# Optimization experiments

Measured on AMD Instinct MI355X. Metric: run time of the kernel, lower is better.

The kernel has to match this reference:

```python
import jax, jax.numpy as jnp
import numpy as np
import math

B, S, H, NH, DH, FF, L = 2, 1024, 768, 12, 64, 3072, 4
LN_EPS = 1e-12


def _layer_norm(x, g, b):
    m = jnp.mean(x, axis=-1, keepdims=True)
    v = jnp.mean(jnp.square(x - m), axis=-1, keepdims=True)
    return (x - m) * jax.lax.rsqrt(v + LN_EPS) * g + b


def _gelu(x):
    # BERT erf-based gelu: x * 0.5 * (1 + erf(x / sqrt(2)))
    return x * 0.5 * (1.0 + jax.lax.erf(x / jnp.sqrt(jnp.asarray(2.0, x.dtype))))


def setup_inputs() -> dict:
    key = jax.random.key(0)
    ks = jax.random.split(key, 10)
    init = lambda k, shape: (jax.random.normal(k, shape, jnp.float32) * 0.02)
    inp = {
        'x': jax.random.normal(ks[0], (B, S, H), jnp.float32),
        'mask': jax.random.randint(ks[1], (B, S, S), 0, 2).astype(jnp.int32),
        'Wq': init(ks[2], (L, H, H)), 'bq': jnp.zeros((L, H), jnp.float32),
        'Wk': init(ks[3], (L, H, H)), 'bk': jnp.zeros((L, H), jnp.float32),
        'Wv': init(ks[4], (L, H, H)), 'bv': jnp.zeros((L, H), jnp.float32),
        'Wao': init(ks[5], (L, H, H)), 'bao': jnp.zeros((L, H), jnp.float32),
        'g1': jnp.ones((L, H), jnp.float32), 'b1': jnp.zeros((L, H), jnp.float32),
        'Wi': init(ks[6], (L, H, FF)), 'bi': jnp.zeros((L, FF), jnp.float32),
        'Wfo': init(ks[7], (L, FF, H)), 'bfo': jnp.zeros((L, H), jnp.float32),
        'g2': jnp.ones((L, H), jnp.float32), 'b2': jnp.zeros((L, H), jnp.float32),
    }
    return inp


def reference(x, mask, Wq, bq, Wk, bk, Wv, bv, Wao, bao, g1, b1, Wi, bi, Wfo, bfo, g2, b2):
    # additive mask: (1 - mask) * -10000, broadcast over heads -> [B,1,S,S]
    adder = (1.0 - mask.astype(x.dtype))[:, None, :, :] * -10000.0
    scale = 1.0 / math.sqrt(DH)

    def block(h, p):
        (wq, bq_, wk, bk_, wv, bv_, wao, bao_, g1_, b1_, wi, bi_, wfo, bfo_, g2_, b2_) = p
        q = (h @ wq + bq_).reshape(B, S, NH, DH)
        k = (h @ wk + bk_).reshape(B, S, NH, DH)
        v = (h @ wv + bv_).reshape(B, S, NH, DH)
        scores = jnp.einsum('bqhd,bkhd->bhqk', q, k) * scale + adder
        probs = jax.nn.softmax(scores, axis=-1)
        ctx = jnp.einsum('bhqk,bkhd->bqhd', probs, v).reshape(B, S, H)
        attn_out = _layer_norm(ctx @ wao + bao_ + h, g1_, b1_)
        inter = _gelu(attn_out @ wi + bi_)
        out = _layer_norm(inter @ wfo + bfo_ + attn_out, g2_, b2_)
        return out, None

    params = (Wq, bq, Wk, bk, Wv, bv, Wao, bao, g1, b1, Wi, bi, Wfo, bfo, g2, b2)
    out, _ = jax.lax.scan(block, x, params)
    return out
```

## Files before the change

kernel.cpp:

```cpp
#include <hip/hip_runtime.h>
#include <math.h>

#define B_  2
#define S_  1024
#define H_  768
#define NH_ 12
#define DH_ 64
#define FF_ 3072
#define L_  4

typedef short v8s __attribute__((ext_vector_type(8)));
typedef float v4f __attribute__((ext_vector_type(4)));

static __device__ __forceinline__ unsigned short f2bf(float f) {
    unsigned int u = __float_as_uint(f);
    unsigned int r = (u + 0x7fffu + ((u >> 16) & 1u)) >> 16;
    return (unsigned short)r;
}
static __device__ __forceinline__ float bf2f(unsigned short u) {
    return __uint_as_float((unsigned int)u << 16);
}

#define GLOAD16(g, l) __builtin_amdgcn_global_load_lds( \
    (const __attribute__((address_space(1))) unsigned int*)(g), \
    (__attribute__((address_space(3))) unsigned int*)(l), 16, 0, 0)

__global__ void conv_bf16_k(const float* __restrict__ in, unsigned short* __restrict__ out, int n) {
    int i = blockIdx.x * 256 + threadIdx.x;
    if (i < n) out[i] = f2bf(in[i]);
}

__global__ void maskconv_k(const int* __restrict__ m, unsigned short* __restrict__ o, int n) {
    int i = blockIdx.x * 256 + threadIdx.x;
    if (i < n) o[i] = m[i] ? (unsigned short)0u : (unsigned short)0xC61Cu;
}

__global__ __launch_bounds__(256) void transpose_convert(
    const float* __restrict__ W, unsigned short* __restrict__ Wt,
    int K, int N, size_t in_lstride, size_t out_lstride)
{
    __shared__ float tile[32][33];
    const int l = blockIdx.z;
    const float* src = W + (size_t)l * in_lstride;
    unsigned short* dst = Wt + (size_t)l * out_lstride;
    const int k0 = blockIdx.x * 32;
    const int n0 = blockIdx.y * 32;
    const int t = threadIdx.x;
    const int tc = t & 31, tr = t >> 5;
#pragma unroll
    for (int i = 0; i < 4; ++i) {
        int r = tr + i * 8;
        tile[r][tc] = src[(size_t)(k0 + r) * N + n0 + tc];
    }
    __syncthreads();
#pragma unroll
    for (int i = 0; i < 4; ++i) {
        int r = tr + i * 8;
        dst[(size_t)(n0 + r) * K + k0 + tc] = f2bf(tile[tc][r]);
    }
}

template<int ACT, int OUT_BF, int NBIAS, int SPLIT>
__global__ __launch_bounds__(256) void gemm_k(
    const unsigned short* __restrict__ A,
    const unsigned short* __restrict__ Bt,
    const float* __restrict__ b0,
    const float* __restrict__ b1,
    const float* __restrict__ b2,
    const float* __restrict__ res,
    void* __restrict__ out0,
    float* __restrict__ out1,
    int M, int N, int K, int klen)
{
    __shared__ __align__(16) unsigned short As[2][128 * 64];
    __shared__ __align__(16) unsigned short Bs[2][64 * 64];
    const int t = threadIdx.x;
    const int m0 = blockIdx.x * 128;
    const int n0 = blockIdx.y * 64;
    const int kz = SPLIT ? blockIdx.z : 0;
    const int kstart = kz * klen;
    const int lane = t & 63;
    const int w = t >> 6;
    const int wm = w >> 1, wn = w & 1;
    const int l15 = lane & 15;
    const int q4  = lane >> 4;

    const unsigned short* gA[4];
    const unsigned short* gB[2];
#pragma unroll
    for (int i = 0; i < 4; ++i) {
        int c = t + i * 256;
        int r = c >> 3, cc = c & 7;
        gA[i] = A + (size_t)(m0 + r) * K + kstart + ((cc ^ (r & 7)) << 3);
    }
#pragma unroll
    for (int i = 0; i < 2; ++i) {
        int c = t + i * 256;
        int r = c >> 3, cc = c & 7;
        gB[i] = Bt + (size_t)(n0 + r) * K + kstart + ((cc ^ (r & 7)) << 3);
    }
    const int ldsW = w * 512;

    v4f acc[4][2] = {};
    const int nt = klen >> 6;

#pragma unroll
    for (int i = 0; i < 4; ++i) GLOAD16(gA[i], &As[0][i * 2048 + ldsW]);
#pragma unroll
    for (int i = 0; i < 2; ++i) GLOAD16(gB[i], &Bs[0][i * 2048 + ldsW]);

    int cur = 0;
    for (int kt = 0; kt < nt; ++kt) {
        __syncthreads();
        if (kt + 1 < nt) {
            const size_t go = (size_t)(kt + 1) << 6;
#pragma unroll
            for (int i = 0; i < 4; ++i) GLOAD16(gA[i] + go, &As[cur ^ 1][i * 2048 + ldsW]);
#pragma unroll
            for (int i = 0; i < 2; ++i) GLOAD16(gB[i] + go, &Bs[cur ^ 1][i * 2048 + ldsW]);
        }
        const unsigned short* as = As[cur];
        const unsigned short* bs = Bs[cur];
#pragma unroll
        for (int ks = 0; ks < 2; ++ks) {
            v8s af[4], bf[2];
#pragma unroll
            for (int i = 0; i < 4; ++i) {
                int r = wm * 64 + i * 16 + l15;
                af[i] = *(const v8s*)&as[r * 64 + ((((ks << 2) + q4) ^ (r & 7)) << 3)];
            }
#pragma unroll
            for (int i = 0; i < 2; ++i) {
                int r = wn * 32 + i * 16 + l15;
                bf[i] = *(const v8s*)&bs[r * 64 + ((((ks << 2) + q4) ^ (r & 7)) << 3)];
            }
#pragma unroll
            for (int fm = 0; fm < 4; ++fm)
#pragma unroll
                for (int fn = 0; fn < 2; ++fn)
                    acc[fm][fn] = __builtin_amdgcn_mfma_f32_16x16x32_bf16(af[fm], bf[fn], acc[fm][fn], 0, 0, 0);
        }
        cur ^= 1;
    }

    const int rb = q4 * 4;
#pragma unroll
    for (int fm = 0; fm < 4; ++fm)
#pragma unroll
        for (int fn = 0; fn < 2; ++fn)
#pragma unroll
            for (int i = 0; i < 4; ++i) {
                const int row = m0 + wm * 64 + fm * 16 + rb + i;
                const int col = n0 + wn * 32 + fn * 16 + l15;
                float v = acc[fm][fn][i];
                const size_t oi = (size_t)row * N + col;
                if (!SPLIT || kz == 0) {
                    float bb;
                    if (NBIAS == 3) {
                        int which = (col >= 1536) ? 2 : (col >= 768 ? 1 : 0);
                        const float* bp = (which == 0) ? b0 : ((which == 1) ? b1 : b2);
                        bb = bp[col - which * 768];
                    } else {
                        bb = b0[col];
                    }
                    v += bb;
                    if (res) v += res[oi];
                    if (ACT == 1) v = 0.5f * v * (1.0f + erff(v * 0.70710678118654752f));
                    if (OUT_BF) ((unsigned short*)out0)[oi] = f2bf(v);
                    else        ((float*)out0)[oi] = v;
                } else {
                    out1[oi] = v;
                }
            }
}

__global__ __launch_bounds__(256) void ln_k(
    const float* __restrict__ ina, const float* __restrict__ inb,
    const float* __restrict__ g, const float* __restrict__ be,
    float* __restrict__ outf, unsigned short* __restrict__ outb)
{
    const int row = blockIdx.x;
    const float* xa = ina + (size_t)row * H_;
    const float* xb = inb + (size_t)row * H_;
    const int t = threadIdx.x;
    const int wave = t >> 6, lane = t & 63;
    float v0 = xa[t] + xb[t];
    float v1 = xa[t + 256] + xb[t + 256];
    float v2 = xa[t + 512] + xb[t + 512];
    float s = v0 + v1 + v2;
    float s2 = v0 * v0 + v1 * v1 + v2 * v2;
#pragma unroll
    for (int o = 32; o; o >>= 1) { s += __shfl_xor(s, o); s2 += __shfl_xor(s2, o); }
    __shared__ float rs[4], rq[4];
    if (lane == 0) { rs[wave] = s; rq[wave] = s2; }
    __syncthreads();
    s  = rs[0] + rs[1] + rs[2] + rs[3];
    s2 = rq[0] + rq[1] + rq[2] + rq[3];
    const float mean = s * (1.0f / 768.0f);
    float var = s2 * (1.0f / 768.0f) - mean * mean;
    var = fmaxf(var, 0.0f);
    const float inv = rsqrtf(var + 1e-12f);
#pragma unroll
    for (int i = 0; i < 3; ++i) {
        int c = t + i * 256;
        float vv = (i == 0) ? v0 : ((i == 1) ? v1 : v2);
        float y = (vv - mean) * inv * g[c] + be[c];
        outf[(size_t)row * H_ + c] = y;
        outb[(size_t)row * H_ + c] = f2bf(y);
    }
}

__global__ __launch_bounds__(512) void fattn_k(
    const unsigned short* __restrict__ qkv,
    const unsigned short* __restrict__ madd,
    unsigned short* __restrict__ ctx)
{
    const int qt = blockIdx.x, h = blockIdx.y, b = blockIdx.z;
    const int q0 = qt * 64;
    const int t = threadIdx.x;
    const int w = t >> 6, lane = t & 63;
    const int half = w >> 2, w4 = w & 3;
    const int l15 = lane & 15;
    const int kr8 = (lane >> 4) * 8;
    const int rb  = (lane >> 4) * 4;
    const int wq0 = w4 * 16;

    __shared__ __align__(16) unsigned char smem[53248];
    unsigned short* KsH = (unsigned short*)(smem)         + (size_t)half * (64 * 72);
    unsigned short* VtH = (unsigned short*)(smem + 18432) + (size_t)half * 4096;
    unsigned short* PsH = (unsigned short*)(smem + 34816) + (size_t)half * (64 * 72);

    const size_t rstr = 2304;
    const unsigned short* base = qkv + (size_t)b * S_ * rstr + h * 64;

    v8s qf0, qf1;
    {
        const unsigned short* qp = base + (size_t)(q0 + wq0 + l15) * rstr + kr8;
        qf0 = *(const v8s*)qp;
        qf1 = *(const v8s*)(qp + 32);
    }

    const int tl  = t & 255;
    const int skp = tl >> 3;
    const int sd0 = (tl & 7) * 8;
    const unsigned short* kbase = base + 768  + (size_t)(half * 512 + skp) * rstr + sd0;
    const unsigned short* vbase = base + 1536 + (size_t)(half * 512 + 2 * skp) * rstr + sd0;
    const size_t kstep = (size_t)64 * rstr;

    float m_[4], l_[4];
    v4f accO[4];
#pragma unroll
    for (int i = 0; i < 4; ++i) { m_[i] = -3.0e38f; l_[i] = 0.f; }
#pragma unroll
    for (int f = 0; f < 4; ++f) accO[f] = (v4f){0.f, 0.f, 0.f, 0.f};

    const unsigned short* mrow[4];
#pragma unroll
    for (int i = 0; i < 4; ++i)
        mrow[i] = madd + ((size_t)(b * S_) + q0 + wq0 + rb + i) * S_ + half * 512;

    v8s kA0, kA1, vA0, vA1, kB0, kB1, vB0, vB1;
    kA0 = *(const v8s*)(kbase);
    kA1 = *(const v8s*)(kbase + 32 * rstr);
    vA0 = *(const v8s*)(vbase);
    vA1 = *(const v8s*)(vbase + rstr);

    for (int kt = 0; kt < 8; ++kt) {
        const int k0 = kt * 64;
        __syncthreads();
        if ((kt & 1) == 0) {
            *(v8s*)&KsH[skp * 72 + sd0] = kA0;
            *(v8s*)&KsH[(skp + 32) * 72 + sd0] = kA1;
#pragma unroll
            for (int j = 0; j < 8; ++j) {
                const int d = sd0 + j;
                const int sw = ((d & 7) ^ (d >> 3)) << 3;
                unsigned int pk = ((unsigned int)(unsigned short)vA1[j] << 16) | (unsigned short)vA0[j];
                *(unsigned int*)&VtH[(size_t)d * 64 + ((2 * skp) ^ sw)] = pk;
            }
            if (kt < 7) {
                const unsigned short* kp = kbase + (size_t)(kt + 1) * kstep;
                const unsigned short* vp = vbase + (size_t)(kt + 1) * kstep;
                kB0 = *(const v8s*)kp;
                kB1 = *(const v8s*)(kp + 32 * rstr);
                vB0 = *(const v8s*)vp;
                vB1 = *(const v8s*)(vp + rstr);
            }
        } else {
            *(v8s*)&KsH[skp * 72 + sd0] = kB0;
            *(v8s*)&KsH[(skp + 32) * 72 + sd0] = kB1;
#pragma unroll
            for (int j = 0; j < 8; ++j) {
                const int d = sd0 + j;
                const int sw = ((d & 7) ^ (d >> 3)) << 3;
                unsigned int pk = ((unsigned int)(unsigned short)vB1[j] << 16) | (unsigned short)vB0[j];
                *(unsigned int*)&VtH[(size_t)d * 64 + ((2 * skp) ^ sw)] = pk;
            }
            if (kt < 7) {
                const unsigned short* kp = kbase + (size_t)(kt + 1) * kstep;
                const unsigned short* vp = vbase + (size_t)(kt + 1) * kstep;
                kA0 = *(const v8s*)kp;
                kA1 = *(const v8s*)(kp + 32 * rstr);
                vA0 = *(const v8s*)vp;
                vA1 = *(const v8s*)(vp + rstr);
            }
        }
        __syncthreads();

        v4f s4[4];
#pragma unroll
        for (int f = 0; f < 4; ++f) s4[f] = (v4f){0.f, 0.f, 0.f, 0.f};
#pragma unroll
        for (int ks = 0; ks < 2; ++ks) {
            v8s qv = ks ? qf1 : qf0;
#pragma unroll
            for (int f = 0; f < 4; ++f) {
                v8s kf = *(const v8s*)&KsH[(f * 16 + l15) * 72 + ks * 32 + kr8];
                s4[f] = __builtin_amdgcn_mfma_f32_16x16x32_bf16(qv, kf, s4[f], 0, 0, 0);
            }
        }

        float p[4][4];
        float mx[4];
#pragma unroll
        for (int i = 0; i < 4; ++i) mx[i] = -3.0e38f;
#pragma unroll
        for (int f = 0; f < 4; ++f)
#pragma unroll
            for (int i = 0; i < 4; ++i) {
                float v = s4[f][i] * 0.125f + bf2f(mrow[i][k0 + f * 16 + l15]);
                p[f][i] = v;
                mx[i] = fmaxf(mx[i], v);
            }
#pragma unroll
        for (int o = 8; o; o >>= 1)
#pragma unroll
            for (int i = 0; i < 4; ++i) mx[i] = fmaxf(mx[i], __shfl_xor(mx[i], o));
        float corr[4], rsum[4];
#pragma unroll
        for (int i = 0; i < 4; ++i) {
            float mn = fmaxf(m_[i], mx[i]);
            corr[i] = __expf(m_[i] - mn);
            m_[i] = mn;
            rsum[i] = 0.f;
        }
#pragma unroll
        for (int f = 0; f < 4; ++f)
#pragma unroll
            for (int i = 0; i < 4; ++i) {
                float e = __expf(p[f][i] - m_[i]);
                p[f][i] = e;
                rsum[i] += e;
            }
#pragma unroll
        for (int o = 8; o; o >>= 1)
#pragma unroll
            for (int i = 0; i < 4; ++i) rsum[i] += __shfl_xor(rsum[i], o);
#pragma unroll
        for (int i = 0; i < 4; ++i) l_[i] = l_[i] * corr[i] + rsum[i];
#pragma unroll
        for (int f = 0; f < 4; ++f)
#pragma unroll
            for (int i = 0; i < 4; ++i) accO[f][i] *= corr[i];

#pragma unroll
        for (int f = 0; f < 4; ++f)
#pragma unroll
            for (int i = 0; i < 4; ++i)
                PsH[(wq0 + rb + i) * 72 + f * 16 + l15] = f2bf(p[f][i]);

#pragma unroll
        for (int ks = 0; ks < 2; ++ks) {
            v8s pf = *(const v8s*)&PsH[(wq0 + l15) * 72 + ks * 32 + kr8];
#pragma unroll
            for (int f = 0; f < 4; ++f) {
                const int d = f * 16 + l15;
                const int sw = ((d & 7) ^ (d >> 3)) << 3;
                v8s vf = *(const v8s*)&VtH[(size_t)d * 64 + ((ks * 32 + kr8) ^ sw)];
                accO[f] = __builtin_amdgcn_mfma_f32_16x16x32_bf16(pf, vf, accO[f], 0, 0, 0);
            }
        }
    }

    __syncthreads();
    float* Mb = (float*)smem;
    const int mstr = 26;
    if (half == 1) {
        float* p = Mb + ((size_t)(w4 * 64 + lane)) * mstr;
#pragma unroll
        for (int i = 0; i < 4; ++i) { p[i] = m_[i]; p[4 + i] = l_[i]; }
#pragma unroll
        for (int f = 0; f < 4; ++f)
#pragma unroll
            for (int i = 0; i < 4; ++i) p[8 + f * 4 + i] = accO[f][i];
    }
    __syncthreads();
    if (half == 0) {
        const float* p = Mb + ((size_t)(w4 * 64 + lane)) * mstr;
        float c0[4], c1[4];
#pragma unroll
        for (int i = 0; i < 4; ++i) {
            float m1 = p[i], l1 = p[4 + i];
            float mm = fmaxf(m_[i], m1);
            c0[i] = __expf(m_[i] - mm);
            c1[i] = __expf(m1 - mm);
            l_[i] = l_[i] * c0[i] + l1 * c1[i];
            m_[i] = mm;
        }
#pragma unroll
        for (int f = 0; f < 4; ++f)
#pragma unroll
            for (int i = 0; i < 4; ++i) {
                float o = (accO[f][i] * c0[i] + p[8 + f * 4 + i] * c1[i]) / l_[i];
                size_t row = (size_t)(b * S_) + q0 + wq0 + rb + i;
                ctx[row * 768 + h * 64 + f * 16 + l15] = f2bf(o);
            }
    }
}

extern "C" void kernel_launch(void* const* d_in, const int* in_sizes, int n_in,
                              void* d_out, int out_size, void* d_ws, size_t ws_size,
                              hipStream_t stream)
{
    const float* x   = (const float*)d_in[0];
    const int*   mask= (const int*)  d_in[1];
    const float* Wq  = (const float*)d_in[2];
    const float* bq  = (const float*)d_in[3];
    const float* Wk  = (const float*)d_in[4];
    const float* bk  = (const float*)d_in[5];
    const float* Wv  = (const float*)d_in[6];
    const float* bv  = (const float*)d_in[7];
    const float* Wao = (const float*)d_in[8];
    const float* bao = (const float*)d_in[9];
    const float* g1  = (const float*)d_in[10];
    const float* b1  = (const float*)d_in[11];
    const float* Wi  = (const float*)d_in[12];
    const float* bi  = (const float*)d_in[13];
    const float* Wfo = (const float*)d_in[14];
    const float* bfo = (const float*)d_in[15];
    const float* g2  = (const float*)d_in[16];
    const float* b2  = (const float*)d_in[17];
    float* out = (float*)d_out;

    const int M = B_ * S_;
    char* basep = (char*)d_ws;
    size_t off = 0;
    auto alloc = [&](size_t bytes) -> char* {
        char* p = basep + off;
        off = (off + bytes + 255) & ~(size_t)255;
        return p;
    };

    unsigned short* WqkvT = (unsigned short*)alloc((size_t)L_ * 2304 * 768 * 2);
    unsigned short* WaoT  = (unsigned short*)alloc((size_t)L_ * 768 * 768 * 2);
    unsigned short* WiT   = (unsigned short*)alloc((size_t)L_ * 3072 * 768 * 2);
    unsigned short* WfoT  = (unsigned short*)alloc((size_t)L_ * 768 * 3072 * 2);
    unsigned short* h_bf  = (unsigned short*)alloc((size_t)M * 768 * 2);
    unsigned short* qkvbf = (unsigned short*)alloc((size_t)M * 2304 * 2);
    unsigned short* ctxbf = (unsigned short*)alloc((size_t)M * 768 * 2);
    float* t1a            = (float*)alloc((size_t)M * 768 * 4);
    float* attnf          = (float*)alloc((size_t)M * 768 * 4);
    unsigned short* attnbf= (unsigned short*)alloc((size_t)M * 768 * 2);
    unsigned short* interbf = (unsigned short*)alloc((size_t)M * FF_ * 2);
    unsigned short* madd  = (unsigned short*)alloc((size_t)B_ * S_ * S_ * 2);
    float* t1b = (float*)(void*)qkvbf;

    dim3 tb(256);
    transpose_convert<<<dim3(24, 24, L_), tb, 0, stream>>>(Wq,  WqkvT + 0,          768,  768, (size_t)768 * 768,  (size_t)2304 * 768);
    transpose_convert<<<dim3(24, 24, L_), tb, 0, stream>>>(Wk,  WqkvT + 768 * 768,  768,  768, (size_t)768 * 768,  (size_t)2304 * 768);
    transpose_convert<<<dim3(24, 24, L_), tb, 0, stream>>>(Wv,  WqkvT + 1536 * 768, 768,  768, (size_t)768 * 768,  (size_t)2304 * 768);
    transpose_convert<<<dim3(24, 24, L_), tb, 0, stream>>>(Wao, WaoT,               768,  768, (size_t)768 * 768,  (size_t)768 * 768);
    transpose_convert<<<dim3(24, 96, L_), tb, 0, stream>>>(Wi,  WiT,                768, 3072, (size_t)768 * 3072, (size_t)3072 * 768);
    transpose_convert<<<dim3(96, 24, L_), tb, 0, stream>>>(Wfo, WfoT,              3072,  768, (size_t)3072 * 768, (size_t)768 * 3072);

    conv_bf16_k<<<(M * 768 + 255) / 256, 256, 0, stream>>>(x, h_bf, M * 768);
    maskconv_k<<<(B_ * S_ * S_ + 255) / 256, 256, 0, stream>>>(mask, madd, B_ * S_ * S_);

    const float* hres = x;
    for (int l = 0; l < L_; ++l) {
        gemm_k<0, 1, 3, 0><<<dim3(16, 36), tb, 0, stream>>>(
            h_bf, WqkvT + (size_t)l * 2304 * 768,
            bq + l * 768, bk + l * 768, bv + l * 768, nullptr, qkvbf, nullptr, M, 2304, 768, 768);
        fattn_k<<<dim3(S_ / 64, NH_, B_), dim3(512), 0, stream>>>(qkvbf, madd, ctxbf);
        gemm_k<0, 0, 1, 1><<<dim3(16, 12, 2), tb, 0, stream>>>(
            ctxbf, WaoT + (size_t)l * 768 * 768,
            bao + l * 768, nullptr, nullptr, hres, t1a, t1b, M, 768, 768, 384);
        ln_k<<<M, tb, 0, stream>>>(t1a, t1b, g1 + l * 768, b1 + l * 768, attnf, attnbf);
        gemm_k<1, 1, 1, 0><<<dim3(16, 48), tb, 0, stream>>>(
            attnbf, WiT + (size_t)l * 3072 * 768,
            bi + l * 3072, nullptr, nullptr, nullptr, interbf, nullptr, M, 3072, 768, 768);
        gemm_k<0, 0, 1, 1><<<dim3(16, 12, 2), tb, 0, stream>>>(
            interbf, WfoT + (size_t)l * 3072 * 768,
            bfo + l * 768, nullptr, nullptr, attnf, t1a, t1b, M, 768, 3072, 1536);
        ln_k<<<M, tb, 0, stream>>>(t1a, t1b, g2 + l * 768, b2 + l * 768, out, h_bf);
        hres = out;
    }
}
```

Before: 768.8 us.

## Split attention KV range across blocks and merge partials in separate kernel

The fused attention kernel drops from 512-thread blocks, which merged two KV halves through shared memory, to 256-thread blocks. Each block now handles one KV half and writes unnormalized fp32 partial outputs plus max/sum stats to scratch buffers, which a new merge kernel combines into bf16 context. The softmax moves to base-2: scores are scaled by log2(e)/8, the mask constant is rescaled to match, and exp2f is used. Mask values are also preloaded ahead of the barrier. This trades an extra launch and fp32 partial traffic for more, smaller blocks and less shared memory per block, which should raise occupancy.

After: 734.1 us. -4.5%, faster.

```diff
diff --git a/kernel.cpp b/kernel.cpp
--- a/kernel.cpp
+++ b/kernel.cpp
@@ -32,7 +32,7 @@
 
 __global__ void maskconv_k(const int* __restrict__ m, unsigned short* __restrict__ o, int n) {
     int i = blockIdx.x * 256 + threadIdx.x;
-    if (i < n) o[i] = m[i] ? (unsigned short)0u : (unsigned short)0xC61Cu;
+    if (i < n) o[i] = m[i] ? (unsigned short)0u : (unsigned short)0xC661u;
 }
 
 __global__ __launch_bounds__(256) void transpose_convert(
@@ -210,25 +210,25 @@
     }
 }
 
-__global__ __launch_bounds__(512) void fattn_k(
+__global__ __launch_bounds__(256) void fattn_k(
     const unsigned short* __restrict__ qkv,
     const unsigned short* __restrict__ madd,
-    unsigned short* __restrict__ ctx)
+    float* __restrict__ pO,
+    float* __restrict__ pML)
 {
-    const int qt = blockIdx.x, h = blockIdx.y, b = blockIdx.z;
+    const int qt = blockIdx.x, h = blockIdx.y, zz = blockIdx.z;
+    const int b = zz >> 1, kvh = zz & 1;
     const int q0 = qt * 64;
     const int t = threadIdx.x;
     const int w = t >> 6, lane = t & 63;
-    const int half = w >> 2, w4 = w & 3;
     const int l15 = lane & 15;
     const int kr8 = (lane >> 4) * 8;
     const int rb  = (lane >> 4) * 4;
-    const int wq0 = w4 * 16;
-
-    __shared__ __align__(16) unsigned char smem[53248];
-    unsigned short* KsH = (unsigned short*)(smem)         + (size_t)half * (64 * 72);
-    unsigned short* VtH = (unsigned short*)(smem + 18432) + (size_t)half * 4096;
-    unsigned short* PsH = (unsigned short*)(smem + 34816) + (size_t)half * (64 * 72);
+    const int wq0 = w * 16;
+
+    __shared__ __align__(16) unsigned short Ks[64][72];
+    __shared__ __align__(16) unsigned short Vt[4096];
+    __shared__ __align__(16) unsigned short Ps[64][72];
 
     const size_t rstr = 2304;
     const unsigned short* base = qkv + (size_t)b * S_ * rstr + h * 64;
@@ -240,11 +240,10 @@
         qf1 = *(const v8s*)(qp + 32);
     }
 
-    const int tl  = t & 255;
-    const int skp = tl >> 3;
-    const int sd0 = (tl & 7) * 8;
-    const unsigned short* kbase = base + 768  + (size_t)(half * 512 + skp) * rstr + sd0;
-    const unsigned short* vbase = base + 1536 + (size_t)(half * 512 + 2 * skp) * rstr + sd0;
+    const int skp = t >> 3;
+    const int sd0 = (t & 7) * 8;
+    const unsigned short* kbase = base + 768  + (size_t)(kvh * 512 + skp) * rstr + sd0;
+    const unsigned short* vbase = base + 1536 + (size_t)(kvh * 512 + 2 * skp) * rstr + sd0;
     const size_t kstep = (size_t)64 * rstr;
 
     float m_[4], l_[4];
@@ -257,7 +256,7 @@
     const unsigned short* mrow[4];
 #pragma unroll
     for (int i = 0; i < 4; ++i)
-        mrow[i] = madd + ((size_t)(b * S_) + q0 + wq0 + rb + i) * S_ + half * 512;
+        mrow[i] = madd + ((size_t)(b * S_) + q0 + wq0 + rb + i) * S_ + kvh * 512;
 
     v8s kA0, kA1, vA0, vA1, kB0, kB1, vB0, vB1;
     kA0 = *(const v8s*)(kbase);
@@ -265,18 +264,27 @@
     vA0 = *(const v8s*)(vbase);
     vA1 = *(const v8s*)(vbase + rstr);
 
+    const float SC2 = 0.18033688011112042f;
+
     for (int kt = 0; kt < 8; ++kt) {
         const int k0 = kt * 64;
+        unsigned short mu[16];
+#pragma unroll
+        for (int f = 0; f < 4; ++f)
+#pragma unroll
+            for (int i = 0; i < 4; ++i)
+                mu[f * 4 + i] = mrow[i][k0 + f * 16 + l15];
+
         __syncthreads();
         if ((kt & 1) == 0) {
-            *(v8s*)&KsH[skp * 72 + sd0] = kA0;
-            *(v8s*)&KsH[(skp + 32) * 72 + sd0] = kA1;
+            *(v8s*)&Ks[skp][sd0] = kA0;
+            *(v8s*)&Ks[skp + 32][sd0] = kA1;
 #pragma unroll
             for (int j = 0; j < 8; ++j) {
                 const int d = sd0 + j;
                 const int sw = ((d & 7) ^ (d >> 3)) << 3;
                 unsigned int pk = ((unsigned int)(unsigned short)vA1[j] << 16) | (unsigned short)vA0[j];
-                *(unsigned int*)&VtH[(size_t)d * 64 + ((2 * skp) ^ sw)] = pk;
+                *(unsigned int*)&Vt[(size_t)d * 64 + ((2 * skp) ^ sw)] = pk;
             }
             if (kt < 7) {
                 const unsigned short* kp = kbase + (size_t)(kt + 1) * kstep;
@@ -287,14 +295,14 @@
                 vB1 = *(const v8s*)(vp + rstr);
             }
         } else {
-            *(v8s*)&KsH[skp * 72 + sd0] = kB0;
-            *(v8s*)&KsH[(skp + 32) * 72 + sd0] = kB1;
+            *(v8s*)&Ks[skp][sd0] = kB0;
+            *(v8s*)&Ks[skp + 32][sd0] = kB1;
 #pragma unroll
             for (int j = 0; j < 8; ++j) {
                 const int d = sd0 + j;
                 const int sw = ((d & 7) ^ (d >> 3)) << 3;
                 unsigned int pk = ((unsigned int)(unsigned short)vB1[j] << 16) | (unsigned short)vB0[j];
-                *(unsigned int*)&VtH[(size_t)d * 64 + ((2 * skp) ^ sw)] = pk;
+                *(unsigned int*)&Vt[(size_t)d * 64 + ((2 * skp) ^ sw)] = pk;
             }
             if (kt < 7) {
                 const unsigned short* kp = kbase + (size_t)(kt + 1) * kstep;
@@ -315,7 +323,7 @@
             v8s qv = ks ? qf1 : qf0;
 #pragma unroll
             for (int f = 0; f < 4; ++f) {
-                v8s kf = *(const v8s*)&KsH[(f * 16 + l15) * 72 + ks * 32 + kr8];
+                v8s kf = *(const v8s*)&Ks[f * 16 + l15][ks * 32 + kr8];
                 s4[f] = __builtin_amdgcn_mfma_f32_16x16x32_bf16(qv, kf, s4[f], 0, 0, 0);
             }
         }
@@ -328,7 +336,7 @@
         for (int f = 0; f < 4; ++f)
 #pragma unroll
             for (int i = 0; i < 4; ++i) {
-                float v = s4[f][i] * 0.125f + bf2f(mrow[i][k0 + f * 16 + l15]);
+                float v = s4[f][i] * SC2 + bf2f(mu[f * 4 + i]);
                 p[f][i] = v;
                 mx[i] = fmaxf(mx[i], v);
             }
@@ -340,7 +348,7 @@
 #pragma unroll
         for (int i = 0; i < 4; ++i) {
             float mn = fmaxf(m_[i], mx[i]);
-            corr[i] = __expf(m_[i] - mn);
+            corr[i] = exp2f(m_[i] - mn);
             m_[i] = mn;
             rsum[i] = 0.f;
         }
@@ -348,7 +356,7 @@
         for (int f = 0; f < 4; ++f)
 #pragma unroll
             for (int i = 0; i < 4; ++i) {
-                float e = __expf(p[f][i] - m_[i]);
+                float e = exp2f(p[f][i] - m_[i]);
                 p[f][i] = e;
                 rsum[i] += e;
             }
@@ -367,55 +375,64 @@
         for (int f = 0; f < 4; ++f)
 #pragma unroll
             for (int i = 0; i < 4; ++i)
-                PsH[(wq0 + rb + i) * 72 + f * 16 + l15] = f2bf(p[f][i]);
+                Ps[wq0 + rb + i][f * 16 + l15] = f2bf(p[f][i]);
 
 #pragma unroll
         for (int ks = 0; ks < 2; ++ks) {
-            v8s pf = *(const v8s*)&PsH[(wq0 + l15) * 72 + ks * 32 + kr8];
+            v8s pf = *(const v8s*)&Ps[wq0 + l15][ks * 32 + kr8];
 #pragma unroll
             for (int f = 0; f < 4; ++f) {
                 const int d = f * 16 + l15;
                 const int sw = ((d & 7) ^ (d >> 3)) << 3;
-                v8s vf = *(const v8s*)&VtH[(size_t)d * 64 + ((ks * 32 + kr8) ^ sw)];
+                v8s vf = *(const v8s*)&Vt[(size_t)d * 64 + ((ks * 32 + kr8) ^ sw)];
                 accO[f] = __builtin_amdgcn_mfma_f32_16x16x32_bf16(pf, vf, accO[f], 0, 0, 0);
             }
         }
     }
 
-    __syncthreads();
-    float* Mb = (float*)smem;
-    const int mstr = 26;
-    if (half == 1) {
-        float* p = Mb + ((size_t)(w4 * 64 + lane)) * mstr;
-#pragma unroll
-        for (int i = 0; i < 4; ++i) { p[i] = m_[i]; p[4 + i] = l_[i]; }
-#pragma unroll
-        for (int f = 0; f < 4; ++f)
-#pragma unroll
-            for (int i = 0; i < 4; ++i) p[8 + f * 4 + i] = accO[f][i];
-    }
-    __syncthreads();
-    if (half == 0) {
-        const float* p = Mb + ((size_t)(w4 * 64 + lane)) * mstr;
-        float c0[4], c1[4];
+    float* po = pO + (size_t)kvh * (2048 * 768);
+#pragma unroll
+    for (int f = 0; f < 4; ++f)
 #pragma unroll
         for (int i = 0; i < 4; ++i) {
-            float m1 = p[i], l1 = p[4 + i];
-            float mm = fmaxf(m_[i], m1);
-            c0[i] = __expf(m_[i] - mm);
-            c1[i] = __expf(m1 - mm);
-            l_[i] = l_[i] * c0[i] + l1 * c1[i];
-            m_[i] = mm;
-        }
-#pragma unroll
-        for (int f = 0; f < 4; ++f)
-#pragma unroll
-            for (int i = 0; i < 4; ++i) {
-                float o = (accO[f][i] * c0[i] + p[8 + f * 4 + i] * c1[i]) / l_[i];
-                size_t row = (size_t)(b * S_) + q0 + wq0 + rb + i;
-                ctx[row * 768 + h * 64 + f * 16 + l15] = f2bf(o);
-            }
-    }
+            size_t row = (size_t)(b * S_) + q0 + wq0 + rb + i;
+            po[row * 768 + h * 64 + f * 16 + l15] = accO[f][i];
+        }
+    if (l15 == 0) {
+#pragma unroll
+        for (int i = 0; i < 4; ++i) {
+            size_t row = (size_t)(b * S_) + q0 + wq0 + rb + i;
+            size_t idx = (((size_t)kvh * 2048 + row) * NH_ + h) * 2;
+            pML[idx] = m_[i];
+            pML[idx + 1] = l_[i];
+        }
+    }
+}
+
+__global__ __launch_bounds__(256) void attn_merge(
+    const float* __restrict__ pO, const float* __restrict__ pML,
+    unsigned short* __restrict__ ctx)
+{
+    const int i = blockIdx.x * 256 + threadIdx.x;
+    const int row = i / 192;
+    const int c4 = (i - row * 192) * 4;
+    const int h = c4 >> 6;
+    const size_t mi0 = ((size_t)row * NH_ + h) * 2;
+    const size_t mi1 = (((size_t)2048 + row) * NH_ + h) * 2;
+    const float m0 = pML[mi0], l0 = pML[mi0 + 1];
+    const float m1 = pML[mi1], l1 = pML[mi1 + 1];
+    const float mm = fmaxf(m0, m1);
+    const float c0 = exp2f(m0 - mm), c1 = exp2f(m1 - mm);
+    const float inv = 1.0f / (l0 * c0 + l1 * c1);
+    const size_t off = (size_t)row * 768 + c4;
+    float4 o0 = *(const float4*)&pO[off];
+    float4 o1 = *(const float4*)&pO[(size_t)2048 * 768 + off];
+    unsigned short r[4];
+    r[0] = f2bf((o0.x * c0 + o1.x * c1) * inv);
+    r[1] = f2bf((o0.y * c0 + o1.y * c1) * inv);
+    r[2] = f2bf((o0.z * c0 + o1.z * c1) * inv);
+    r[3] = f2bf((o0.w * c0 + o1.w * c1) * inv);
+    *(uint2*)&ctx[off] = *(uint2*)r;
 }
 
 extern "C" void kernel_launch(void* const* d_in, const int* in_sizes, int n_in,
@@ -464,6 +481,8 @@
     unsigned short* interbf = (unsigned short*)alloc((size_t)M * FF_ * 2);
     unsigned short* madd  = (unsigned short*)alloc((size_t)B_ * S_ * S_ * 2);
     float* t1b = (float*)(void*)qkvbf;
+    float* pO  = (float*)(void*)interbf;
+    float* pML = t1a;
 
     dim3 tb(256);
     transpose_convert<<<dim3(24, 24, L_), tb, 0, stream>>>(Wq,  WqkvT + 0,          768,  768, (size_t)768 * 768,  (size_t)2304 * 768);
@@ -481,7 +500,8 @@
         gemm_k<0, 1, 3, 0><<<dim3(16, 36), tb, 0, stream>>>(
             h_bf, WqkvT + (size_t)l * 2304 * 768,
             bq + l * 768, bk + l * 768, bv + l * 768, nullptr, qkvbf, nullptr, M, 2304, 768, 768);
-        fattn_k<<<dim3(S_ / 64, NH_, B_), dim3(512), 0, stream>>>(qkvbf, madd, ctxbf);
+        fattn_k<<<dim3(S_ / 64, NH_, B_ * 2), tb, 0, stream>>>(qkvbf, madd, pO, pML);
+        attn_merge<<<1536, tb, 0, stream>>>(pO, pML, ctxbf);
         gemm_k<0, 0, 1, 1><<<dim3(16, 12, 2), tb, 0, stream>>>(
             ctxbf, WaoT + (size_t)l * 768 * 768,
             bao + l * 768, nullptr, nullptr, hres, t1a, t1b, M, 768, 768, 384);
```
